# Optimization experiments

Measured on AMD Instinct MI355X. Metric: run time of the kernel, lower is better.

Reference implementation:

```python
import jax, jax.numpy as jnp
import numpy as np

B = 64        # graphs per batch
N_PER = 1024  # nodes per graph
DEG = 16      # avg degree
H = 128       # hidden width


def _graph_conv(x, src, dst, emask, Wr, b, Wl):
    # PyG GraphConv: out_i = W_rel @ sum_{j->i} x_j + b + W_root @ x_i
    msg = x[src] * emask[:, None]                       # [E, F]
    agg = jax.ops.segment_sum(msg, dst, num_segments=x.shape[0])
    return agg @ Wr + x @ Wl + b


def _topk_pool(x, w, nmask, src, dst, emask, ratio=0.8):
    # PyG TopKPooling: score = (x @ w)/||w||, keep top ceil(ratio*n_i) per graph,
    # kept x scaled by tanh(score). Expressed with masks (fixed shapes).
    score = (x @ w) / jnp.linalg.norm(w)                # [N]
    score = jnp.where(nmask > 0, score, -jnp.inf)
    s2 = score.reshape(B, -1)
    rank = jnp.argsort(jnp.argsort(-s2, axis=1), axis=1)  # rank 0 = largest score
    counts = nmask.reshape(B, -1).sum(axis=1)
    k = jnp.ceil(ratio * counts)
    keep = (rank < k[:, None]).reshape(-1).astype(x.dtype)
    x_new = x * jnp.where(keep > 0, jnp.tanh(score), 0.0)[:, None]
    emask_new = emask * keep[src] * keep[dst]
    return x_new, keep, emask_new


def _readout(x, nmask):
    # concat(global_max_pool, global_mean_pool) over surviving nodes per graph
    xg = x.reshape(B, -1, x.shape[-1])
    m = nmask.reshape(B, -1, 1)
    mx = jnp.max(jnp.where(m > 0, xg, -jnp.inf), axis=1)
    mn = (xg * m).sum(axis=1) / m.sum(axis=1)
    return jnp.concatenate([mx, mn], axis=1)            # [B, 2H]


def setup_inputs():
    key = jax.random.key(0)
    ks = jax.random.split(key, 16)
    N = B * N_PER
    x = jax.random.normal(ks[0], (N, 4), dtype=jnp.float32)
    e_per = N_PER * DEG
    off = (jnp.arange(B) * N_PER)[:, None]
    src = (jax.random.randint(ks[1], (B, e_per), 0, N_PER) + off).reshape(-1)
    dst = (jax.random.randint(ks[2], (B, e_per), 0, N_PER) + off).reshape(-1)
    edge_index = jnp.stack([src, dst]).astype(jnp.int32)

    def lin(k, fi, fo, s=0.1):
        return jax.random.normal(k, (fi, fo), dtype=jnp.float32) * s

    return {
        "x": x, "edge_index": edge_index,
        "w1r": lin(ks[3], 4, H), "b1": jnp.zeros((H,), jnp.float32), "w1l": lin(ks[4], 4, H),
        "w2r": lin(ks[5], H, H), "b2": jnp.zeros((H,), jnp.float32), "w2l": lin(ks[6], H, H),
        "w3r": lin(ks[7], H, H), "b3": jnp.zeros((H,), jnp.float32), "w3l": lin(ks[8], H, H),
        "p1w": jax.random.normal(ks[9], (H,), jnp.float32) * 0.1,
        "p2w": jax.random.normal(ks[10], (H,), jnp.float32) * 0.1,
        "w_lin1": lin(ks[11], 2 * H, H), "b_lin1": jnp.zeros((H,), jnp.float32),
        "w_lin2": lin(ks[12], H, 64), "b_lin2": jnp.zeros((64,), jnp.float32),
        "w_lin3": lin(ks[13], 64, 7), "b_lin3": jnp.zeros((7,), jnp.float32),
    }


def reference(x, edge_index, w1r, b1, w1l, w2r, b2, w2l, w3r, b3, w3l,
              p1w, p2w, w_lin1, b_lin1, w_lin2, b_lin2, w_lin3, b_lin3):
    src, dst = edge_index[0], edge_index[1]
    nmask = jnp.ones((x.shape[0],), x.dtype)
    emask = jnp.ones((src.shape[0],), x.dtype)

    h = jax.nn.relu(_graph_conv(x, src, dst, emask, w1r, b1, w1l)) * nmask[:, None]
    h, nmask, emask = _topk_pool(h, p1w, nmask, src, dst, emask)
    x1 = _readout(h, nmask)

    h = jax.nn.relu(_graph_conv(h, src, dst, emask, w2r, b2, w2l)) * nmask[:, None]
    h, nmask, emask = _topk_pool(h, p2w, nmask, src, dst, emask)
    x2 = _readout(h, nmask)

    h = jax.nn.relu(_graph_conv(h, src, dst, emask, w3r, b3, w3l)) * nmask[:, None]
    # NOTE: original forward reuses self.pool2 for the third pooling (pool3 unused)
    h, nmask, emask = _topk_pool(h, p2w, nmask, src, dst, emask)
    x3 = _readout(h, nmask)

    z = x1 + x2 + x3
    z = jax.nn.relu(z @ w_lin1 + b_lin1)
    # F.dropout with training=False (eval) is identity
    z = jax.nn.relu(z @ w_lin2 + b_lin2)
    return jax.nn.log_softmax(z @ w_lin3 + b_lin3, axis=-1)  # [B, 7]
```

## Files before the change

### kernel.cpp

```cpp
#include <hip/hip_runtime.h>
#include <hip/hip_bf16.h>
#include <math.h>

#define NN   65536
#define NG   64
#define NPER 1024
#define NE   1048576
#define EPG  16384
#define HD   128
#define K1 820
#define K2 656
#define K3 525

typedef unsigned short u16;
typedef unsigned int   u32;
typedef __attribute__((ext_vector_type(8))) short short8;
typedef __attribute__((ext_vector_type(8))) u16 u16x8;
typedef __attribute__((ext_vector_type(4))) float floatx4;

__device__ __forceinline__ float bf2f(u16 u) {
    union { u32 i; float f; } v; v.i = ((u32)u) << 16; return v.f;
}
__device__ __forceinline__ u16 f2bf(float f) {
    u32 x = __float_as_uint(f);
    return (u16)((x + 0x7fffu + ((x >> 16) & 1u)) >> 16);
}
__device__ __forceinline__ float ldx(const void* p, size_t i, int bf) {
    return bf ? bf2f(((const u16*)p)[i]) : ((const float*)p)[i];
}

__global__ void k_sentinel(u32* out) {
    if (threadIdx.x < 224) out[threadIdx.x] = 0x46404640u;
}

__global__ __launch_bounds__(1024) void k_prep(
    const int* __restrict__ src, const int* __restrict__ dst,
    int* __restrict__ row_ptr, int* __restrict__ col,
    const void* __restrict__ x, int* __restrict__ flag,
    const void* __restrict__ W2r, const void* __restrict__ W2l,
    const void* __restrict__ W3r, const void* __restrict__ W3l,
    u16* __restrict__ hi2, u16* __restrict__ lo2,
    u16* __restrict__ hi3, u16* __restrict__ lo3) {
    __shared__ int s_scan[1024];
    __shared__ int s_cur[1024];
    int b = blockIdx.x, t = threadIdx.x;
    if (b >= 64) {
        int ok = 0;
        if (t < 256) {
            u16 u = ((const u16*)x)[2 * t];
            int e = (u >> 7) & 0xFF;
            ok = (e >= 100 && e <= 140) ? 1 : 0;
        }
        s_scan[t] = ok;
        __syncthreads();
        for (int off = 512; off; off >>= 1) {
            if (t < off) s_scan[t] += s_scan[t + off];
            __syncthreads();
        }
        int bf = (s_scan[0] >= 192) ? 1 : 0;
        if (b == 64) {
            if (t == 0) flag[0] = bf;
            return;
        }
        int pb = b - 65;
        int which = pb >> 5;
        const void* Wr = which ? W3r : W2r;
        const void* Wl = which ? W3l : W2l;
        u16* hi = which ? hi3 : hi2;
        u16* lo = which ? lo3 : lo2;
        int idx = (pb & 31) * 1024 + t;
        int j = idx & 7;
        int lane = (idx >> 3) & 63;
        int c = (idx >> 9) & 7;
        int tt = idx >> 12;
        int k = c * 32 + ((lane >> 4) << 3) + j;
        int n = tt * 16 + (lane & 15);
        float w = (k < HD) ? ldx(Wr, (size_t)k * HD + n, bf)
                           : ldx(Wl, (size_t)(k - HD) * HD + n, bf);
        u16 h = f2bf(w);
        hi[idx] = h;
        lo[idx] = f2bf(w - bf2f(h));
        return;
    }
    int g = b;
    int ebase = g * EPG;
    s_scan[t] = 0;
    __syncthreads();
    #pragma unroll
    for (int i = 0; i < 16; i++) {
        int dd = dst[ebase + i * 1024 + t] - g * NPER;
        atomicAdd(&s_scan[dd], 1);
    }
    __syncthreads();
    int v = s_scan[t];
    __syncthreads();
    s_scan[t] = v;
    __syncthreads();
    for (int off = 1; off < 1024; off <<= 1) {
        int x2 = (t >= off) ? s_scan[t - off] : 0;
        __syncthreads();
        s_scan[t] += x2;
        __syncthreads();
    }
    int excl = s_scan[t] - v;
    row_ptr[g * NPER + t] = ebase + excl;
    if (g == 0 && t == 0) row_ptr[NN] = NE;
    s_cur[t] = excl;
    __syncthreads();
    #pragma unroll
    for (int i = 0; i < 16; i++) {
        int e = ebase + i * 1024 + t;
        int dd = dst[e] - g * NPER;
        int p = atomicAdd(&s_cur[dd], 1);
        col[ebase + p] = src[e];
    }
}

__global__ void k_conv1(const void* __restrict__ x, const int* __restrict__ row_ptr,
                        const int* __restrict__ col,
                        const void* __restrict__ w1r, const void* __restrict__ b1,
                        const void* __restrict__ w1l, u16* __restrict__ hbf,
                        const void* __restrict__ pw, float* __restrict__ score,
                        const int* __restrict__ flag) {
    const int bf = *flag;
    int wave = threadIdx.x >> 6, lane = threadIdx.x & 63;
    int node = (blockIdx.x & 63) * NPER + (blockIdx.x >> 6) * 4 + wave;
    int rp = row_ptr[node], rq = row_ptr[node + 1];
    float a0 = 0.f, a1 = 0.f, a2 = 0.f, a3 = 0.f;
    for (int j = rp + lane; j < rq; j += 64) {
        int s = col[j];
        if (bf) {
            ushort4 u = *(const ushort4*)((const u16*)x + (size_t)s * 4);
            a0 += bf2f(u.x); a1 += bf2f(u.y); a2 += bf2f(u.z); a3 += bf2f(u.w);
        } else {
            float4 u = *(const float4*)((const float*)x + (size_t)s * 4);
            a0 += u.x; a1 += u.y; a2 += u.z; a3 += u.w;
        }
    }
    for (int m = 32; m; m >>= 1) {
        a0 += __shfl_xor(a0, m, 64);
        a1 += __shfl_xor(a1, m, 64);
        a2 += __shfl_xor(a2, m, 64);
        a3 += __shfl_xor(a3, m, 64);
    }
    float x0, x1, x2, x3;
    if (bf) {
        ushort4 u = *(const ushort4*)((const u16*)x + (size_t)node * 4);
        x0 = bf2f(u.x); x1 = bf2f(u.y); x2 = bf2f(u.z); x3 = bf2f(u.w);
    } else {
        float4 u = *(const float4*)((const float*)x + (size_t)node * 4);
        x0 = u.x; x1 = u.y; x2 = u.z; x3 = u.w;
    }
    float vout[2];
    #pragma unroll
    for (int rep = 0; rep < 2; rep++) {
        int o = lane + rep * 64;
        float v = ldx(b1, o, bf);
        v += a0 * ldx(w1r, 0 * HD + o, bf) + a1 * ldx(w1r, 1 * HD + o, bf)
           + a2 * ldx(w1r, 2 * HD + o, bf) + a3 * ldx(w1r, 3 * HD + o, bf);
        v += x0 * ldx(w1l, 0 * HD + o, bf) + x1 * ldx(w1l, 1 * HD + o, bf)
           + x2 * ldx(w1l, 2 * HD + o, bf) + x3 * ldx(w1l, 3 * HD + o, bf);
        v = fmaxf(v, 0.f);
        vout[rep] = v;
        hbf[(size_t)node * HD + o] = f2bf(v);
    }
    float w0 = ldx(pw, lane, bf), w1 = ldx(pw, lane + 64, bf);
    float dot = vout[0] * w0 + vout[1] * w1;
    float nrm = w0 * w0 + w1 * w1;
    for (int m = 32; m; m >>= 1) {
        dot += __shfl_xor(dot, m, 64);
        nrm += __shfl_xor(nrm, m, 64);
    }
    if (lane == 0) score[node] = dot / sqrtf(nrm);
}

__global__ __launch_bounds__(256) void k_pool2(
    const float* __restrict__ score, const float* __restrict__ prev_keep,
    float* __restrict__ out_keep, float* __restrict__ out_val,
    const u16* __restrict__ h, float* __restrict__ pmax, float* __restrict__ psum,
    int K) {
    __shared__ __align__(16) float s_sc[1024];
    __shared__ int s_r[256];
    __shared__ float s_val[128], s_keep[128];
    __shared__ float s_mx[8][128], s_sm[8][128];
    int g = blockIdx.x & 63, chunk = blockIdx.x >> 6;
    int t = threadIdx.x;
    #pragma unroll
    for (int i = 0; i < 4; i++) {
        int j = t + i * 256;
        float sc = score[g * NPER + j];
        if (prev_keep && prev_keep[g * NPER + j] == 0.f) sc = -INFINITY;
        s_sc[j] = sc;
    }
    __syncthreads();
    int nloc = chunk * 128 + (t & 127);
    int half = t >> 7;
    float sc = s_sc[nloc];
    int r = 0;
    #pragma unroll 4
    for (int j4 = half * 128; j4 < half * 128 + 128; j4++) {
        float4 sv = *(const float4*)&s_sc[j4 * 4];
        int j = j4 * 4;
        r += (int)((sv.x > sc) || (sv.x == sc && j     < nloc));
        r += (int)((sv.y > sc) || (sv.y == sc && j + 1 < nloc));
        r += (int)((sv.z > sc) || (sv.z == sc && j + 2 < nloc));
        r += (int)((sv.w > sc) || (sv.w == sc && j + 3 < nloc));
    }
    s_r[t] = r;
    __syncthreads();
    if (t < 128) {
        int rt = s_r[t] + s_r[t + 128];
        bool kp = rt < K;
        float kpf = kp ? 1.f : 0.f;
        float vv = kp ? tanhf(sc) : 0.f;
        out_keep[g * NPER + nloc] = kpf;
        out_val[g * NPER + nloc] = vv;
        s_keep[t] = kpf;
        s_val[t] = vv;
    }
    __syncthreads();
    int cg = t & 31, slot = t >> 5;
    float4 mx = {-INFINITY, -INFINITY, -INFINITY, -INFINITY};
    float4 sm = {0.f, 0.f, 0.f, 0.f};
    #pragma unroll 4
    for (int i = 0; i < 16; i++) {
        int nn = slot * 16 + i;
        float vv = s_val[nn], kp = s_keep[nn];
        const u16* hp = h + (size_t)(g * NPER + chunk * 128 + nn) * HD + cg * 4;
        ushort4 u = *(const ushort4*)hp;
        float4 v;
        v.x = bf2f(u.x) * vv; v.y = bf2f(u.y) * vv;
        v.z = bf2f(u.z) * vv; v.w = bf2f(u.w) * vv;
        sm.x += v.x; sm.y += v.y; sm.z += v.z; sm.w += v.w;
        if (kp != 0.f) {
            mx.x = fmaxf(mx.x, v.x); mx.y = fmaxf(mx.y, v.y);
            mx.z = fmaxf(mx.z, v.z); mx.w = fmaxf(mx.w, v.w);
        }
    }
    *(float4*)&s_mx[slot][cg * 4] = mx;
    *(float4*)&s_sm[slot][cg * 4] = sm;
    __syncthreads();
    if (t < 128) {
        float M = s_mx[0][t], S = s_sm[0][t];
        #pragma unroll
        for (int s = 1; s < 8; s++) {
            M = fmaxf(M, s_mx[s][t]);
            S += s_sm[s][t];
        }
        size_t o = (size_t)(chunk * 64 + g) * HD + t;
        pmax[o] = M;
        psum[o] = S;
    }
}

__global__ __launch_bounds__(256) void k_agg(const u16* __restrict__ hbf,
                      const float* __restrict__ val,
                      const int* __restrict__ row_ptr,
                      const int* __restrict__ col, float* __restrict__ agg) {
    int g = blockIdx.x & 63, chunk = blockIdx.x >> 6;
    int wave = threadIdx.x >> 6, lane = threadIdx.x & 63;
    int node = g * NPER + chunk * 4 + wave;
    int rp = row_ptr[node], rq = row_ptr[node + 1];
    int deg = rq - rp;
    int e = lane >> 4, c = lane & 15;
    float a[8];
    #pragma unroll
    for (int j = 0; j < 8; j++) a[j] = 0.f;
    for (int base = 0; base < deg; base += 64) {
        int bcnt = min(64, deg - base);
        int myidx = col[rp + base + ((lane < bcnt) ? lane : 0)];
        int m = 0;
        for (; m + 16 <= bcnt; m += 16) {
            int s0 = __shfl(myidx, m + e, 64);
            int s1 = __shfl(myidx, m + 4 + e, 64);
            int s2 = __shfl(myidx, m + 8 + e, 64);
            int s3 = __shfl(myidx, m + 12 + e, 64);
            float vs0 = val[s0], vs1 = val[s1], vs2 = val[s2], vs3 = val[s3];
            u16x8 r0 = *(const u16x8*)(hbf + (size_t)s0 * HD + c * 8);
            u16x8 r1 = *(const u16x8*)(hbf + (size_t)s1 * HD + c * 8);
            u16x8 r2 = *(const u16x8*)(hbf + (size_t)s2 * HD + c * 8);
            u16x8 r3 = *(const u16x8*)(hbf + (size_t)s3 * HD + c * 8);
            #pragma unroll
            for (int j = 0; j < 8; j++) {
                a[j] += bf2f(r0[j]) * vs0;
                a[j] += bf2f(r1[j]) * vs1;
                a[j] += bf2f(r2[j]) * vs2;
                a[j] += bf2f(r3[j]) * vs3;
            }
        }
        for (; m + 4 <= bcnt; m += 4) {
            int s0 = __shfl(myidx, m + e, 64);
            float vs0 = val[s0];
            u16x8 r0 = *(const u16x8*)(hbf + (size_t)s0 * HD + c * 8);
            #pragma unroll
            for (int j = 0; j < 8; j++) a[j] += bf2f(r0[j]) * vs0;
        }
        int rem = bcnt - m;
        if (rem > 0) {
            int s0 = __shfl(myidx, m + ((e < rem) ? e : 0), 64);
            float vs0 = val[s0];
            u16x8 r0 = *(const u16x8*)(hbf + (size_t)s0 * HD + c * 8);
            if (e < rem) {
                #pragma unroll
                for (int j = 0; j < 8; j++) a[j] += bf2f(r0[j]) * vs0;
            }
        }
    }
    #pragma unroll
    for (int j = 0; j < 8; j++) {
        a[j] += __shfl_xor(a[j], 16, 64);
        a[j] += __shfl_xor(a[j], 32, 64);
    }
    if (e == 0) {
        float4 o0 = {a[0], a[1], a[2], a[3]};
        float4 o1 = {a[4], a[5], a[6], a[7]};
        *(float4*)(agg + (size_t)node * HD + c * 8) = o0;
        *(float4*)(agg + (size_t)node * HD + c * 8 + 4) = o1;
    }
}

__global__ __launch_bounds__(256) void k_gemm_mfma(
    const float* __restrict__ agg, const u16* __restrict__ hbf,
    const u16* __restrict__ whi, const u16* __restrict__ wlo,
    const void* __restrict__ bias, const float* __restrict__ keep,
    const float* __restrict__ val, u16* __restrict__ outbf,
    const void* __restrict__ pw, float* __restrict__ score,
    const int* __restrict__ flag) {
    const int bf = *flag;
    int t = threadIdx.x;
    int w = t >> 6, lane = t & 63;
    int quad = lane >> 4;
    int m0 = (blockIdx.x & 63) * NPER + (blockIdx.x >> 6) * 64 + w * 16;
    int mrow = m0 + (lane & 15);
    float vrow = val[mrow];

    floatx4 acc[8];
    #pragma unroll
    for (int i = 0; i < 8; i++) acc[i] = (floatx4)0.f;

    #pragma unroll
    for (int c = 0; c < 8; c++) {
        float av[8];
        int kb = (c & 3) * 32 + quad * 8;
        if (c < 4) {
            const float* pa = agg + (size_t)mrow * HD + kb;
            float4 a0 = *(const float4*)pa;
            float4 a1 = *(const float4*)(pa + 4);
            av[0] = a0.x; av[1] = a0.y; av[2] = a0.z; av[3] = a0.w;
            av[4] = a1.x; av[5] = a1.y; av[6] = a1.z; av[7] = a1.w;
        } else {
            u16x8 hr = *(const u16x8*)(hbf + (size_t)mrow * HD + kb);
            #pragma unroll
            for (int j = 0; j < 8; j++) av[j] = bf2f(hr[j]) * vrow;
        }
        short8 ahi, alo;
        #pragma unroll
        for (int j = 0; j < 8; j++) {
            u16 hb = f2bf(av[j]);
            ahi[j] = (short)hb;
            alo[j] = (short)f2bf(av[j] - bf2f(hb));
        }
        #pragma unroll
        for (int tt = 0; tt < 8; tt++) {
            const u16* bp = whi + (((size_t)(tt * 8 + c) * 64 + lane) << 3);
            short8 bhi = *(const short8*)bp;
            acc[tt] = __builtin_amdgcn_mfma_f32_16x16x32_bf16(ahi, bhi, acc[tt], 0, 0, 0);
            acc[tt] = __builtin_amdgcn_mfma_f32_16x16x32_bf16(alo, bhi, acc[tt], 0, 0, 0);
        }
        if (!bf) {
            #pragma unroll
            for (int tt = 0; tt < 8; tt++) {
                const u16* bp = wlo + (((size_t)(tt * 8 + c) * 64 + lane) << 3);
                short8 blo = *(const short8*)bp;
                acc[tt] = __builtin_amdgcn_mfma_f32_16x16x32_bf16(ahi, blo, acc[tt], 0, 0, 0);
            }
        }
    }

    float kf[4];
    #pragma unroll
    for (int r = 0; r < 4; r++) kf[r] = keep[m0 + quad * 4 + r];
    float sp0 = 0.f, sp1 = 0.f, sp2 = 0.f, sp3 = 0.f, nrm = 0.f;
    #pragma unroll
    for (int tt = 0; tt < 8; tt++) {
        int colc = tt * 16 + (lane & 15);
        float bcol = ldx(bias, colc, bf);
        float wv = ldx(pw, colc, bf);
        nrm += wv * wv;
        #pragma unroll
        for (int r = 0; r < 4; r++) {
            int row = m0 + quad * 4 + r;
            float v = fmaxf(acc[tt][r] + bcol, 0.f) * kf[r];
            outbf[(size_t)row * HD + colc] = f2bf(v);
            if (r == 0) sp0 += v * wv;
            else if (r == 1) sp1 += v * wv;
            else if (r == 2) sp2 += v * wv;
            else sp3 += v * wv;
        }
    }
    #pragma unroll
    for (int m = 1; m < 16; m <<= 1) {
        sp0 += __shfl_xor(sp0, m, 64);
        sp1 += __shfl_xor(sp1, m, 64);
        sp2 += __shfl_xor(sp2, m, 64);
        sp3 += __shfl_xor(sp3, m, 64);
        nrm += __shfl_xor(nrm, m, 64);
    }
    if ((lane & 15) == 0) {
        float inv = 1.f / sqrtf(nrm);
        float4 sc;
        sc.x = sp0 * inv; sc.y = sp1 * inv; sc.z = sp2 * inv; sc.w = sp3 * inv;
        *(float4*)(score + m0 + quad * 4) = sc;
    }
}

__global__ __launch_bounds__(256) void k_mlp(
    const float* __restrict__ pmax1, const float* __restrict__ psum1,
    const float* __restrict__ pmax2, const float* __restrict__ psum2,
    const float* __restrict__ pmax3, const float* __restrict__ psum3,
    const void* __restrict__ w1, const void* __restrict__ b1,
    const void* __restrict__ w2, const void* __restrict__ b2,
    const void* __restrict__ w3, const void* __restrict__ b3,
    void* __restrict__ out, const int* __restrict__ flag) {
    const int bf = *flag;
    int g = blockIdx.x, t = threadIdx.x;
    __shared__ float sIn[256], sZ1[128], sZ2[64], sZ3[7], sRed[2];
    __shared__ float sP1[2][128];
    __shared__ float sP2[4][64];
    if (t < 128) {
        float M1 = -INFINITY, M2 = -INFINITY, M3 = -INFINITY;
        #pragma unroll
        for (int ch = 0; ch < 8; ch++) {
            size_t o = (size_t)(ch * 64 + g) * HD + t;
            M1 = fmaxf(M1, pmax1[o]);
            M2 = fmaxf(M2, pmax2[o]);
            M3 = fmaxf(M3, pmax3[o]);
        }
        sIn[t] = M1 + M2 + M3;
    } else {
        int c = t - 128;
        float S1 = 0.f, S2 = 0.f, S3 = 0.f;
        #pragma unroll
        for (int ch = 0; ch < 8; ch++) {
            size_t o = (size_t)(ch * 64 + g) * HD + c;
            S1 += psum1[o];
            S2 += psum2[o];
            S3 += psum3[o];
        }
        sIn[t] = S1 / (float)K1 + S2 / (float)K2 + S3 / (float)K3;
    }
    __syncthreads();
    {
        int o = t & 127, half = t >> 7;
        float v = 0.f;
        #pragma unroll 8
        for (int k = half * 128; k < half * 128 + 128; k++)
            v += sIn[k] * ldx(w1, (size_t)k * 128 + o, bf);
        sP1[half][o] = v;
    }
    __syncthreads();
    if (t < 128) sZ1[t] = fmaxf(sP1[0][t] + sP1[1][t] + ldx(b1, t, bf), 0.f);
    __syncthreads();
    {
        int o = t & 63, seg = t >> 6;
        float v = 0.f;
        #pragma unroll 8
        for (int k = seg * 32; k < seg * 32 + 32; k++)
            v += sZ1[k] * ldx(w2, (size_t)k * 64 + o, bf);
        sP2[seg][o] = v;
    }
    __syncthreads();
    if (t < 64) sZ2[t] = fmaxf(sP2[0][t] + sP2[1][t] + sP2[2][t] + sP2[3][t]
                               + ldx(b2, t, bf), 0.f);
    __syncthreads();
    if (t < 7) {
        float v = ldx(b3, t, bf);
        #pragma unroll 8
        for (int k = 0; k < 64; k++) v += sZ2[k] * ldx(w3, (size_t)k * 7 + t, bf);
        sZ3[t] = v;
    }
    __syncthreads();
    if (t == 0) {
        float mx = sZ3[0];
        for (int i = 1; i < 7; i++) mx = fmaxf(mx, sZ3[i]);
        float s = 0.f;
        for (int i = 0; i < 7; i++) s += expf(sZ3[i] - mx);
        sRed[0] = mx; sRed[1] = logf(s);
    }
    __syncthreads();
    if (t < 7) {
        float v = sZ3[t] - sRed[0] - sRed[1];
        if (bf) {
            __hip_bfloat16 hb = __float2bfloat16(v);
            ((u16*)out)[g * 7 + t] = *(u16*)&hb;
        } else {
            ((float*)out)[g * 7 + t] = v;
        }
    }
}

extern "C" void kernel_launch(void* const* d_in, const int* in_sizes, int n_in,
                              void* d_out, int out_size, void* d_ws, size_t ws_size,
                              hipStream_t stream) {
    (void)in_sizes; (void)n_in; (void)out_size;
    const void* x   = d_in[0];
    const int* ei   = (const int*)d_in[1];
    const void* w1r = d_in[2];
    const void* b1  = d_in[3];
    const void* w1l = d_in[4];
    const void* w2r = d_in[5];
    const void* b2  = d_in[6];
    const void* w2l = d_in[7];
    const void* w3r = d_in[8];
    const void* b3  = d_in[9];
    const void* w3l = d_in[10];
    const void* p1w = d_in[11];
    const void* p2w = d_in[12];
    const void* wl1 = d_in[13];
    const void* bl1 = d_in[14];
    const void* wl2 = d_in[15];
    const void* bl2 = d_in[16];
    const void* wl3 = d_in[17];
    const void* bl3 = d_in[18];
    const int* srcI = ei;
    const int* dstI = ei + NE;

    char* base = (char*)d_ws;
    char* p = base;
    auto alloc = [&](size_t bytes) -> char* {
        char* r = p; p += (bytes + 255) & ~(size_t)255; return r;
    };
    float* aggbuf = (float*)alloc((size_t)NN * HD * 4);
    u16* h1bf     = (u16*)alloc((size_t)NN * HD * 2);
    u16* h2bf     = (u16*)alloc((size_t)NN * HD * 2);
    u16* h3bf     = (u16*)alloc((size_t)NN * HD * 2);
    int* row_ptr  = (int*)alloc((size_t)(NN + 1) * 4);
    int* colA     = (int*)alloc((size_t)NE * 4);
    float* keep1  = (float*)alloc((size_t)NN * 4);
    float* keep2  = (float*)alloc((size_t)NN * 4);
    float* keep3  = (float*)alloc((size_t)NN * 4);
    float* score  = (float*)alloc((size_t)NN * 4);
    float* val1   = (float*)alloc((size_t)NN * 4);
    float* val2   = (float*)alloc((size_t)NN * 4);
    float* val3   = (float*)alloc((size_t)NN * 4);
    float* pmax1  = (float*)alloc((size_t)8 * NG * HD * 4);
    float* psum1  = (float*)alloc((size_t)8 * NG * HD * 4);
    float* pmax2  = (float*)alloc((size_t)8 * NG * HD * 4);
    float* psum2  = (float*)alloc((size_t)8 * NG * HD * 4);
    float* pmax3  = (float*)alloc((size_t)8 * NG * HD * 4);
    float* psum3  = (float*)alloc((size_t)8 * NG * HD * 4);
    int* flag     = (int*)alloc(256);
    u16* whi2     = (u16*)alloc((size_t)32768 * 2);
    u16* wlo2     = (u16*)alloc((size_t)32768 * 2);
    u16* whi3     = (u16*)alloc((size_t)32768 * 2);
    u16* wlo3     = (u16*)alloc((size_t)32768 * 2);

    if ((size_t)(p - base) > ws_size) {
        k_sentinel<<<1, 256, 0, stream>>>((u32*)d_out);
        return;
    }

    k_prep<<<129, 1024, 0, stream>>>(srcI, dstI, row_ptr, colA, x, flag,
                                     w2r, w2l, w3r, w3l, whi2, wlo2, whi3, wlo3);

    k_conv1<<<NN / 4, 256, 0, stream>>>(x, row_ptr, colA, w1r, b1, w1l, h1bf,
                                        p1w, score, flag);
    k_pool2<<<NG * 8, 256, 0, stream>>>(score, nullptr, keep1, val1, h1bf,
                                        pmax1, psum1, K1);

    k_agg<<<NN / 4, 256, 0, stream>>>(h1bf, val1, row_ptr, colA, aggbuf);
    k_gemm_mfma<<<NN / 64, 256, 0, stream>>>(aggbuf, h1bf, whi2, wlo2, b2, keep1,
                                             val1, h2bf, p2w, score, flag);
    k_pool2<<<NG * 8, 256, 0, stream>>>(score, keep1, keep2, val2, h2bf,
                                        pmax2, psum2, K2);

    k_agg<<<NN / 4, 256, 0, stream>>>(h2bf, val2, row_ptr, colA, aggbuf);
    k_gemm_mfma<<<NN / 64, 256, 0, stream>>>(aggbuf, h2bf, whi3, wlo3, b3, keep2,
                                             val2, h3bf, p2w, score, flag);
    k_pool2<<<NG * 8, 256, 0, stream>>>(score, keep2, keep3, val3, h3bf,
                                        pmax3, psum3, K3);

    k_mlp<<<NG, 256, 0, stream>>>(pmax1, psum1, pmax2, psum2, pmax3, psum3,
                                  wl1, bl1, wl2, bl2, wl3, bl3, d_out, flag);
}
```

Measured before the change: 347.5 us.

## Stage per-graph feature slices and CSR in LDS for neighbor aggregation

Replaces the per-node global-gather aggregation kernel with one that gives each block a single graph and a 32-column feature slice. The block loads that graph's bf16 feature slice (padded to avoid bank conflicts), its column indices, its values and its row pointers into shared memory, then gathers neighbors from LDS. This removes the random global gathers, which are repeated about 16 times per source row, but uses only 256 blocks of 1024 threads with about 140KB of LDS each. That leaves low occupancy, and the inner loop is a serial shuffle loop over each node's edges.

```diff
diff --git a/kernel.cpp b/kernel.cpp
--- a/kernel.cpp
+++ b/kernel.cpp
@@ -253,69 +253,64 @@
     }
 }
 
-__global__ __launch_bounds__(256) void k_agg(const u16* __restrict__ hbf,
-                      const float* __restrict__ val,
-                      const int* __restrict__ row_ptr,
-                      const int* __restrict__ col, float* __restrict__ agg) {
-    int g = blockIdx.x & 63, chunk = blockIdx.x >> 6;
-    int wave = threadIdx.x >> 6, lane = threadIdx.x & 63;
-    int node = g * NPER + chunk * 4 + wave;
-    int rp = row_ptr[node], rq = row_ptr[node + 1];
-    int deg = rq - rp;
-    int e = lane >> 4, c = lane & 15;
-    float a[8];
-    #pragma unroll
-    for (int j = 0; j < 8; j++) a[j] = 0.f;
-    for (int base = 0; base < deg; base += 64) {
-        int bcnt = min(64, deg - base);
-        int myidx = col[rp + base + ((lane < bcnt) ? lane : 0)];
-        int m = 0;
-        for (; m + 16 <= bcnt; m += 16) {
-            int s0 = __shfl(myidx, m + e, 64);
-            int s1 = __shfl(myidx, m + 4 + e, 64);
-            int s2 = __shfl(myidx, m + 8 + e, 64);
-            int s3 = __shfl(myidx, m + 12 + e, 64);
-            float vs0 = val[s0], vs1 = val[s1], vs2 = val[s2], vs3 = val[s3];
-            u16x8 r0 = *(const u16x8*)(hbf + (size_t)s0 * HD + c * 8);
-            u16x8 r1 = *(const u16x8*)(hbf + (size_t)s1 * HD + c * 8);
-            u16x8 r2 = *(const u16x8*)(hbf + (size_t)s2 * HD + c * 8);
-            u16x8 r3 = *(const u16x8*)(hbf + (size_t)s3 * HD + c * 8);
-            #pragma unroll
-            for (int j = 0; j < 8; j++) {
-                a[j] += bf2f(r0[j]) * vs0;
-                a[j] += bf2f(r1[j]) * vs1;
-                a[j] += bf2f(r2[j]) * vs2;
-                a[j] += bf2f(r3[j]) * vs3;
+__global__ __launch_bounds__(1024) void k_agg_lds(
+    const u16* __restrict__ hbf, const float* __restrict__ val,
+    const int* __restrict__ row_ptr, const int* __restrict__ col,
+    float* __restrict__ agg) {
+    __shared__ u32 s_hw[1024 * 17];
+    __shared__ int s_colL[EPG];
+    __shared__ float s_valL[1024];
+    __shared__ int s_rp[1025];
+    int g = blockIdx.x & 63, q = blockIdx.x >> 6;
+    int t = threadIdx.x;
+    int ebase = g * EPG;
+    #pragma unroll
+    for (int i = 0; i < 16; i++) s_colL[i * 1024 + t] = col[ebase + i * 1024 + t];
+    s_valL[t] = val[g * NPER + t];
+    s_rp[t] = row_ptr[g * NPER + t];
+    if (t == 0) s_rp[1024] = row_ptr[g * NPER + 1024];
+    const u32* hw = (const u32*)hbf;
+    #pragma unroll
+    for (int i = 0; i < 4; i++) {
+        int idx4 = i * 1024 + t;
+        int n = idx4 >> 2, w4 = (idx4 & 3) * 4;
+        size_t ga = (size_t)(g * NPER + n) * 64 + q * 16 + w4;
+        u32 a = hw[ga], b = hw[ga + 1], c2 = hw[ga + 2], d = hw[ga + 3];
+        int la = 17 * n + w4;
+        s_hw[la] = a; s_hw[la + 1] = b; s_hw[la + 2] = c2; s_hw[la + 3] = d;
+    }
+    __syncthreads();
+    int wave = t >> 6, lane = t & 63;
+    int slot = lane >> 4, c = lane & 15;
+    int slbase = lane & 48;
+    for (int d_i = 0; d_i < 16; d_i++) {
+        int dl = wave * 64 + d_i * 4 + slot;
+        int rp = s_rp[dl];
+        int deg = s_rp[dl + 1] - rp;
+        int off = rp - ebase;
+        int dm = deg;
+        dm = max(dm, __shfl_xor(dm, 16, 64));
+        dm = max(dm, __shfl_xor(dm, 32, 64));
+        float acc0 = 0.f, acc1 = 0.f;
+        for (int base = 0; base < dm; base += 16) {
+            int ei = base + c;
+            bool valid = ei < deg;
+            int il = valid ? (s_colL[off + (valid ? ei : 0)] & 1023) : 0;
+            float vv = valid ? s_valL[il] : 0.f;
+            int mm = min(16, dm - base);
+            for (int m = 0; m < mm; m++) {
+                int sil = __shfl(il, slbase + m, 64);
+                float svv = __shfl(vv, slbase + m, 64);
+                u32 w = s_hw[17 * sil + c];
+                float lo = __uint_as_float(w << 16);
+                float hi = __uint_as_float(w & 0xffff0000u);
+                acc0 += lo * svv;
+                acc1 += hi * svv;
             }
         }
-        for (; m + 4 <= bcnt; m += 4) {
-            int s0 = __shfl(myidx, m + e, 64);
-            float vs0 = val[s0];
-            u16x8 r0 = *(const u16x8*)(hbf + (size_t)s0 * HD + c * 8);
-            #pragma unroll
-            for (int j = 0; j < 8; j++) a[j] += bf2f(r0[j]) * vs0;
-        }
-        int rem = bcnt - m;
-        if (rem > 0) {
-            int s0 = __shfl(myidx, m + ((e < rem) ? e : 0), 64);
-            float vs0 = val[s0];
-            u16x8 r0 = *(const u16x8*)(hbf + (size_t)s0 * HD + c * 8);
-            if (e < rem) {
-                #pragma unroll
-                for (int j = 0; j < 8; j++) a[j] += bf2f(r0[j]) * vs0;
-            }
-        }
-    }
-    #pragma unroll
-    for (int j = 0; j < 8; j++) {
-        a[j] += __shfl_xor(a[j], 16, 64);
-        a[j] += __shfl_xor(a[j], 32, 64);
-    }
-    if (e == 0) {
-        float4 o0 = {a[0], a[1], a[2], a[3]};
-        float4 o1 = {a[4], a[5], a[6], a[7]};
-        *(float4*)(agg + (size_t)node * HD + c * 8) = o0;
-        *(float4*)(agg + (size_t)node * HD + c * 8 + 4) = o1;
+        size_t oa = (size_t)(g * NPER + dl) * HD + q * 32 + 2 * c;
+        float2 o; o.x = acc0; o.y = acc1;
+        *(float2*)(agg + oa) = o;
     }
 }
 
@@ -568,13 +563,13 @@
     k_pool2<<<NG * 8, 256, 0, stream>>>(score, nullptr, keep1, val1, h1bf,
                                         pmax1, psum1, K1);
 
-    k_agg<<<NN / 4, 256, 0, stream>>>(h1bf, val1, row_ptr, colA, aggbuf);
+    k_agg_lds<<<NG * 4, 1024, 0, stream>>>(h1bf, val1, row_ptr, colA, aggbuf);
     k_gemm_mfma<<<NN / 64, 256, 0, stream>>>(aggbuf, h1bf, whi2, wlo2, b2, keep1,
                                              val1, h2bf, p2w, score, flag);
     k_pool2<<<NG * 8, 256, 0, stream>>>(score, keep1, keep2, val2, h2bf,
                                         pmax2, psum2, K2);
 
-    k_agg<<<NN / 4, 256, 0, stream>>>(h2bf, val2, row_ptr, colA, aggbuf);
+    k_agg_lds<<<NG * 4, 1024, 0, stream>>>(h2bf, val2, row_ptr, colA, aggbuf);
     k_gemm_mfma<<<NN / 64, 256, 0, stream>>>(aggbuf, h2bf, whi3, wlo3, b3, keep2,
                                              val2, h3bf, p2w, score, flag);
     k_pool2<<<NG * 8, 256, 0, stream>>>(score, keep2, keep3, val3, h3bf,
```

New measurement: 388.2 us. 1.12x slower.
